# Kernel optimization log

Hardware: AMD Instinct MI355X
Metric: run time of the kernel (lower is better)

Reference implementation:

```python
import jax, jax.numpy as jnp
import numpy as np

N_NODES = 1024
IN_FEATURES = 512
N_HEADS = 4
N_HIDDEN = 32  # out_features (128) // n_heads (4)
NEG_SLOPE = 0.2


def setup_inputs() -> dict:
    key = jax.random.key(0)
    k1, k2, k3, k4, k5 = jax.random.split(key, 5)
    h = jax.random.normal(k1, (N_NODES, IN_FEATURES), dtype=jnp.float32)
    adj_mat = jax.random.randint(k2, (N_NODES, N_NODES, 1), 0, 2, dtype=jnp.int32)
    s = 1.0 / np.sqrt(IN_FEATURES)
    W_l = jax.random.uniform(k3, (IN_FEATURES, N_HEADS * N_HIDDEN), jnp.float32, -s, s)
    W_r = jax.random.uniform(k4, (IN_FEATURES, N_HEADS * N_HIDDEN), jnp.float32, -s, s)
    sa = 1.0 / np.sqrt(N_HIDDEN)
    attn_w = jax.random.uniform(k5, (N_HIDDEN,), jnp.float32, -sa, sa)
    return {"h": h, "adj_mat": adj_mat, "W_l": W_l, "W_r": W_r, "attn_w": attn_w}


def reference(h, adj_mat, W_l, W_r, attn_w):
    # GraphAttentionV2Layer forward (eval mode: dropout = identity)
    n = h.shape[0]
    g_l = (h @ W_l).reshape(n, N_HEADS, N_HIDDEN)  # source-side (j)
    g_r = (h @ W_r).reshape(n, N_HEADS, N_HIDDEN)  # dest-side (i)
    # g_sum[i, j, h, f] = g_l[j] + g_r[i]  (repeat / repeat_interleave semantics)
    g_sum = g_l[None, :, :, :] + g_r[:, None, :, :]  # [N, N, H, hid]
    act = jnp.where(g_sum >= 0, g_sum, NEG_SLOPE * g_sum)
    e = jnp.einsum('ijhf,f->ijh', act, attn_w)  # [N, N, H]
    mask = (adj_mat == 0)  # broadcasts [N, N, 1] -> [N, N, H]
    e = jnp.where(mask, -jnp.inf, e)
    a = jax.nn.softmax(e, axis=1)  # softmax over neighbors j
    h_prime = jnp.einsum('ijh,jhf->ihf', a, g_r)  # note: aggregates g_r, per source
    h_prime = h_prime.reshape(n, N_HEADS * N_HIDDEN)  # is_concat=True
    # not output layer -> ELU activation (output dropout is identity in eval)
    out = jnp.where(h_prime > 0, h_prime, jnp.expm1(h_prime))
    return out
```

## Files before the change

### kernel.cpp

```cpp
#include <hip/hip_runtime.h>
#include <math.h>

#define N_NODES 1024
#define IN_F 512
#define N_HEADS 4
#define N_HID 32
#define OUT_F 128
#define GF 256
#define NEG_SLOPE 0.2f

__global__ __launch_bounds__(256, 2) void gat_gemm(
    const float* __restrict__ hmat, const float* __restrict__ Wl,
    const float* __restrict__ Wr, float* __restrict__ gpart,
    float* __restrict__ den)
{
  const int b = blockIdx.x;
  if (b < 16) den[b * 256 + threadIdx.x] = 0.f;
  const int kc = b & 7, ct = (b >> 3) & 3, it = b >> 5;
  const int i0 = it * 64, k0 = kc * 64, cb0 = ct * 64;
  const float* __restrict__ W = (cb0 < 128) ? (Wl + cb0) : (Wr + (cb0 - 128));

  __shared__ float As[16][68];
  __shared__ float Bs[16][64];

  const int tx = threadIdx.x & 15, ty = threadIdx.x >> 4;
  const int ar = threadIdx.x >> 2, ak = (threadIdx.x & 3) * 4;
  const int bk = threadIdx.x >> 4, bc = (threadIdx.x & 15) * 4;

  float4 acc0 = {0.f, 0.f, 0.f, 0.f}, acc1 = acc0, acc2 = acc0, acc3 = acc0;

  float4 av = *(const float4*)(hmat + (size_t)(i0 + ar) * IN_F + k0 + ak);
  float4 bv = *(const float4*)(W + (size_t)(k0 + bk) * OUT_F + bc);

  for (int t = 0; t < 64; t += 16) {
    __syncthreads();
    As[ak + 0][ar] = av.x; As[ak + 1][ar] = av.y;
    As[ak + 2][ar] = av.z; As[ak + 3][ar] = av.w;
    *(float4*)&Bs[bk][bc] = bv;
    __syncthreads();
    if (t < 48) {
      av = *(const float4*)(hmat + (size_t)(i0 + ar) * IN_F + k0 + t + 16 + ak);
      bv = *(const float4*)(W + (size_t)(k0 + t + 16 + bk) * OUT_F + bc);
    }
#pragma unroll
    for (int k = 0; k < 16; ++k) {
      const float4 a  = *(const float4*)&As[k][ty * 4];
      const float4 bb = *(const float4*)&Bs[k][tx * 4];
      acc0.x = fmaf(a.x, bb.x, acc0.x); acc0.y = fmaf(a.x, bb.y, acc0.y);
      acc0.z = fmaf(a.x, bb.z, acc0.z); acc0.w = fmaf(a.x, bb.w, acc0.w);
      acc1.x = fmaf(a.y, bb.x, acc1.x); acc1.y = fmaf(a.y, bb.y, acc1.y);
      acc1.z = fmaf(a.y, bb.z, acc1.z); acc1.w = fmaf(a.y, bb.w, acc1.w);
      acc2.x = fmaf(a.z, bb.x, acc2.x); acc2.y = fmaf(a.z, bb.y, acc2.y);
      acc2.z = fmaf(a.z, bb.z, acc2.z); acc2.w = fmaf(a.z, bb.w, acc2.w);
      acc3.x = fmaf(a.w, bb.x, acc3.x); acc3.y = fmaf(a.w, bb.y, acc3.y);
      acc3.z = fmaf(a.w, bb.z, acc3.z); acc3.w = fmaf(a.w, bb.w, acc3.w);
    }
  }
  const size_t rbase = (size_t)kc * N_NODES + i0 + ty * 4;
  const int cc = cb0 + tx * 4;
  *(float4*)(gpart + (rbase + 0) * GF + cc) = acc0;
  *(float4*)(gpart + (rbase + 1) * GF + cc) = acc1;
  *(float4*)(gpart + (rbase + 2) * GF + cc) = acc2;
  *(float4*)(gpart + (rbase + 3) * GF + cc) = acc3;
}

__global__ __launch_bounds__(256) void gat_reduceWab(
    const float* __restrict__ gpart, const float* __restrict__ attn_w,
    float* __restrict__ g, float* __restrict__ abuf, float* __restrict__ bbuf)
{
  const int tid = threadIdx.x;
  const int l = tid & 63, r = tid >> 6;
  const int row = blockIdx.x * 4 + r;
  const size_t o = (size_t)row * GF + l * 4;
  float4 s = *(const float4*)(gpart + o);
#pragma unroll
  for (int c = 1; c < 8; ++c) {
    const float4 v = *(const float4*)(gpart + (size_t)c * (N_NODES * GF) + o);
    s.x += v.x; s.y += v.y; s.z += v.z; s.w += v.w;
  }
  *(float4*)(g + o) = s;
  const float4 a4 = *(const float4*)(attn_w + (l & 7) * 4);
  float d = 0.6f * (s.x * a4.x + s.y * a4.y + s.z * a4.z + s.w * a4.w);
  d += __shfl_xor(d, 1);
  d += __shfl_xor(d, 2);
  d += __shfl_xor(d, 4);
  if ((l & 7) == 0) {
    const int hq = l >> 3;
    if (hq < 4) abuf[hq * N_NODES + row] = d;
    else        bbuf[(hq - 4) * N_NODES + row] = d;
  }
}

__global__ __launch_bounds__(256, 2) void gat_fused(
    const float* __restrict__ g, const float* __restrict__ abuf,
    const float* __restrict__ bbuf, const float* __restrict__ attn_w,
    const int* __restrict__ adj, float* __restrict__ num_part,
    float* __restrict__ den)
{
  __shared__ float4 gl_s[32 * 32];
  __shared__ float4 gr_s[32 * 32];
  __shared__ float as_[4 * 33];

  const int b = blockIdx.x;
  const int jc = b & 7, it = b >> 3;
  const int i0 = it * 16, j0 = jc * 128;

  const int tid = threadIdx.x;
  const int jg = tid & 3, hh = (tid >> 2) & 3, il = tid >> 4;
  const int i = i0 + il;

  const int srow = tid >> 3, sf4 = tid & 7, sjg = srow >> 3;

  float4 gr_i[8], c2[8];
#pragma unroll
  for (int f4 = 0; f4 < 8; ++f4) {
    gr_i[f4] = *(const float4*)(g + (size_t)i * GF + 128 + hh * N_HID + f4 * 4);
    const float4 a4 = *(const float4*)(attn_w + f4 * 4);
    c2[f4] = make_float4(0.4f * a4.x, 0.4f * a4.y, 0.4f * a4.z, 0.4f * a4.w);
  }
  const float beta = bbuf[hh * N_NODES + i];

  int slot[8], wslot[4];
#pragma unroll
  for (int f4 = 0; f4 < 8; ++f4) slot[f4] = hh * 8 + ((f4 + jg + 2 * hh) & 7);
#pragma unroll
  for (int q = 0; q < 4; ++q) wslot[q] = q * 8 + ((sf4 + sjg + 2 * q) & 7);

  float4 pgl[4], pgr[4];
  float pa = 0.f;
  {
    const float* gsrc = g + (size_t)(j0 + srow) * GF;
#pragma unroll
    for (int q = 0; q < 4; ++q) {
      pgl[q] = *(const float4*)(gsrc + (sf4 + 8 * q) * 4);
      pgr[q] = *(const float4*)(gsrc + 128 + (sf4 + 8 * q) * 4);
    }
    if (tid < 128) pa = abuf[(tid >> 5) * N_NODES + j0 + (tid & 31)];
  }

  float4 num4[8];
#pragma unroll
  for (int f4 = 0; f4 < 8; ++f4) num4[f4] = make_float4(0.f, 0.f, 0.f, 0.f);
  float den_t = 0.f;

  for (int t = 0; t < 4; ++t) {
    __syncthreads();
#pragma unroll
    for (int q = 0; q < 4; ++q) {
      gl_s[srow * 32 + wslot[q]] = pgl[q];
      gr_s[srow * 32 + wslot[q]] = pgr[q];
    }
    if (tid < 128) as_[(tid >> 5) * 33 + (tid & 31)] = pa;
    __syncthreads();
    if (t < 3) {
      const float* gs2 = g + (size_t)(j0 + (t + 1) * 32 + srow) * GF;
#pragma unroll
      for (int q = 0; q < 4; ++q) {
        pgl[q] = *(const float4*)(gs2 + (sf4 + 8 * q) * 4);
        pgr[q] = *(const float4*)(gs2 + 128 + (sf4 + 8 * q) * 4);
      }
      if (tid < 128) pa = abuf[(tid >> 5) * N_NODES + j0 + (t + 1) * 32 + (tid & 31)];
    }
    const int4 ad0 = *(const int4*)(adj + (size_t)i * N_NODES + j0 + t * 32 + jg * 8);
    const int4 ad1 = *(const int4*)(adj + (size_t)i * N_NODES + j0 + t * 32 + jg * 8 + 4);
    const int* adp0 = (const int*)&ad0;
    const int* adp1 = (const int*)&ad1;

#pragma unroll
    for (int jj = 0; jj < 8; ++jj) {
      const int jl = jg * 8 + jj;
      const float4* glrow = &gl_s[jl * 32];
      const float4* grrow = &gr_s[jl * 32];
      float4 a0 = make_float4(0.f, 0.f, 0.f, 0.f), a1 = a0;
#pragma unroll
      for (int f4 = 0; f4 < 8; f4 += 2) {
        const float4 v0 = glrow[slot[f4]];
        const float4 v1 = glrow[slot[f4 + 1]];
        float sx, sy, sz, sw;
        sx = v0.x + gr_i[f4].x; sy = v0.y + gr_i[f4].y;
        sz = v0.z + gr_i[f4].z; sw = v0.w + gr_i[f4].w;
        a0.x = fmaf(c2[f4].x, __builtin_fabsf(sx), a0.x);
        a0.y = fmaf(c2[f4].y, __builtin_fabsf(sy), a0.y);
        a0.z = fmaf(c2[f4].z, __builtin_fabsf(sz), a0.z);
        a0.w = fmaf(c2[f4].w, __builtin_fabsf(sw), a0.w);
        sx = v1.x + gr_i[f4 + 1].x; sy = v1.y + gr_i[f4 + 1].y;
        sz = v1.z + gr_i[f4 + 1].z; sw = v1.w + gr_i[f4 + 1].w;
        a1.x = fmaf(c2[f4 + 1].x, __builtin_fabsf(sx), a1.x);
        a1.y = fmaf(c2[f4 + 1].y, __builtin_fabsf(sy), a1.y);
        a1.z = fmaf(c2[f4 + 1].z, __builtin_fabsf(sz), a1.z);
        a1.w = fmaf(c2[f4 + 1].w, __builtin_fabsf(sw), a1.w);
      }
      float e = ((a0.x + a0.y) + (a0.z + a0.w)) + ((a1.x + a1.y) + (a1.z + a1.w));
      e += as_[hh * 33 + jl] + beta;
      float p = __expf(e);
      const int am = (jj < 4) ? adp0[jj] : adp1[jj - 4];
      p = am ? p : 0.f;
      den_t += p;
#pragma unroll
      for (int f4 = 0; f4 < 8; ++f4) {
        const float4 gv = grrow[slot[f4]];
        num4[f4].x = fmaf(p, gv.x, num4[f4].x);
        num4[f4].y = fmaf(p, gv.y, num4[f4].y);
        num4[f4].z = fmaf(p, gv.z, num4[f4].z);
        num4[f4].w = fmaf(p, gv.w, num4[f4].w);
      }
    }
  }

#pragma unroll
  for (int m = 1; m < 4; m <<= 1) {
    den_t += __shfl_xor(den_t, m);
#pragma unroll
    for (int f4 = 0; f4 < 8; ++f4) {
      num4[f4].x += __shfl_xor(num4[f4].x, m);
      num4[f4].y += __shfl_xor(num4[f4].y, m);
      num4[f4].z += __shfl_xor(num4[f4].z, m);
      num4[f4].w += __shfl_xor(num4[f4].w, m);
    }
  }
  if (jg == 0) {
    float* np = num_part + ((size_t)jc * N_NODES + i) * OUT_F + hh * N_HID;
#pragma unroll
    for (int f4 = 0; f4 < 8; ++f4) *(float4*)(np + f4 * 4) = num4[f4];
    atomicAdd(&den[hh * N_NODES + i], den_t);
  }
}

__global__ __launch_bounds__(256) void gat_fin(
    const float* __restrict__ num_part, const float* __restrict__ den,
    float* __restrict__ outp)
{
  const int flat = blockIdx.x * 256 + threadIdx.x;
  const int i = flat >> 7, hf = flat & 127, hh = hf >> 5;
  float t[8];
#pragma unroll
  for (int c = 0; c < 8; ++c)
    t[c] = num_part[(size_t)c * (N_NODES * OUT_F) + flat];
  float s = ((t[0] + t[1]) + (t[2] + t[3])) + ((t[4] + t[5]) + (t[6] + t[7]));
  float v = s / den[hh * N_NODES + i];
  outp[flat] = v > 0.f ? v : expm1f(v);
}

extern "C" void kernel_launch(void* const* d_in, const int* in_sizes, int n_in,
                              void* d_out, int out_size, void* d_ws, size_t ws_size,
                              hipStream_t stream) {
  const float* hmat  = (const float*)d_in[0];
  const int*   adj   = (const int*)d_in[1];
  const float* Wl    = (const float*)d_in[2];
  const float* Wr    = (const float*)d_in[3];
  const float* attnw = (const float*)d_in[4];
  float* outp = (float*)d_out;

  char* ws = (char*)d_ws;
  float* gpart = (float*)(ws);
  float* g     = (float*)(ws + (8u << 20));
  float* den   = (float*)(ws + (9u << 20));
  float* abuf  = (float*)(ws + (9u << 20) + (64u << 10));
  float* bbuf  = (float*)(ws + (9u << 20) + (128u << 10));
  float* npart = (float*)(ws + (10u << 20));

  gat_gemm<<<512, 256, 0, stream>>>(hmat, Wl, Wr, gpart, den);
  gat_reduceWab<<<256, 256, 0, stream>>>(gpart, attnw, g, abuf, bbuf);
  gat_fused<<<512, 256, 0, stream>>>(g, abuf, bbuf, attnw, adj, npart, den);
  gat_fin<<<512, 256, 0, stream>>>(npart, den, outp);
}
```

Before: 126.3 us.

## Pack adjacency into bitmasks and restructure fused attention tiling with per-chunk denominators

Adds a pre-pass that packs the int32 adjacency matrix into 64-bit ballot bitmasks, so the fused kernel reads one word per row chunk instead of int4 loads. The fused kernel is retiled to 32 rows by 64 columns across 16 column chunks. Each thread now covers half of one head's features, with a cross-lane shuffle to complete the score. Denominator atomics are replaced by per-chunk partial sums reduced in the final kernel, which removes the zeroing from the GEMM. The cost is an extra kernel launch and doubled partial-numerator traffic in the finalize step.

```diff
diff --git a/kernel.cpp b/kernel.cpp
--- a/kernel.cpp
+++ b/kernel.cpp
@@ -9,13 +9,25 @@
 #define GF 256
 #define NEG_SLOPE 0.2f
 
+__global__ __launch_bounds__(256) void gat_pack(
+    const int* __restrict__ adj, unsigned long long* __restrict__ bits)
+{
+  const int i = blockIdx.x;
+  const int t = threadIdx.x;
+#pragma unroll
+  for (int q = 0; q < 4; ++q) {
+    const int j = q * 256 + t;
+    const int a = adj[(size_t)i * N_NODES + j];
+    const unsigned long long m = __ballot(a != 0);
+    if ((t & 63) == 0) bits[i * 16 + (j >> 6)] = m;
+  }
+}
+
 __global__ __launch_bounds__(256, 2) void gat_gemm(
     const float* __restrict__ hmat, const float* __restrict__ Wl,
-    const float* __restrict__ Wr, float* __restrict__ gpart,
-    float* __restrict__ den)
+    const float* __restrict__ Wr, float* __restrict__ gpart)
 {
   const int b = blockIdx.x;
-  if (b < 16) den[b * 256 + threadIdx.x] = 0.f;
   const int kc = b & 7, ct = (b >> 3) & 3, it = b >> 5;
   const int i0 = it * 64, k0 = kc * 64, cb0 = ct * 64;
   const float* __restrict__ W = (cb0 < 128) ? (Wl + cb0) : (Wr + (cb0 - 128));
@@ -92,152 +104,111 @@
 }
 
 __global__ __launch_bounds__(256, 2) void gat_fused(
-    const float* __restrict__ g, const float* __restrict__ abuf,
-    const float* __restrict__ bbuf, const float* __restrict__ attn_w,
-    const int* __restrict__ adj, float* __restrict__ num_part,
-    float* __restrict__ den)
-{
-  __shared__ float4 gl_s[32 * 32];
-  __shared__ float4 gr_s[32 * 32];
-  __shared__ float as_[4 * 33];
+    const float* __restrict__ g, const float* __restrict__ attn_w,
+    const float* __restrict__ abuf, const float* __restrict__ bbuf,
+    const unsigned long long* __restrict__ bits,
+    float* __restrict__ num_part, float* __restrict__ den_part)
+{
+  __shared__ float T[32 * 132];
+  __shared__ float as_[4 * 17];
 
   const int b = blockIdx.x;
-  const int jc = b & 7, it = b >> 3;
-  const int i0 = it * 16, j0 = jc * 128;
-
-  const int tid = threadIdx.x;
-  const int jg = tid & 3, hh = (tid >> 2) & 3, il = tid >> 4;
+  const int jc = b & 15, it = b >> 4;
+  const int i0 = it * 32, j0 = jc * 64;
+
+  const int t = threadIdx.x;
+  const int hh = t >> 6, half = (t >> 5) & 1, il = t & 31;
   const int i = i0 + il;
-
-  const int srow = tid >> 3, sf4 = tid & 7, sjg = srow >> 3;
-
-  float4 gr_i[8], c2[8];
-#pragma unroll
-  for (int f4 = 0; f4 < 8; ++f4) {
-    gr_i[f4] = *(const float4*)(g + (size_t)i * GF + 128 + hh * N_HID + f4 * 4);
-    const float4 a4 = *(const float4*)(attn_w + f4 * 4);
-    c2[f4] = make_float4(0.4f * a4.x, 0.4f * a4.y, 0.4f * a4.z, 0.4f * a4.w);
+  const int fbase = hh * N_HID + half * 16;
+
+  float4 gri[4], c2[4], num4[4];
+#pragma unroll
+  for (int q = 0; q < 4; ++q) {
+    gri[q] = *(const float4*)(g + (size_t)i * GF + 128 + fbase + q * 4);
+    const float4 a4 = *(const float4*)(attn_w + half * 16 + q * 4);
+    c2[q] = make_float4(0.4f * a4.x, 0.4f * a4.y, 0.4f * a4.z, 0.4f * a4.w);
+    num4[q] = make_float4(0.f, 0.f, 0.f, 0.f);
   }
   const float beta = bbuf[hh * N_NODES + i];
-
-  int slot[8], wslot[4];
-#pragma unroll
-  for (int f4 = 0; f4 < 8; ++f4) slot[f4] = hh * 8 + ((f4 + jg + 2 * hh) & 7);
-#pragma unroll
-  for (int q = 0; q < 4; ++q) wslot[q] = q * 8 + ((sf4 + sjg + 2 * q) & 7);
-
-  float4 pgl[4], pgr[4];
-  float pa = 0.f;
+  const unsigned long long bm = bits[(size_t)i * 16 + jc];
+  float den_t = 0.f;
+
+  const int sr = t >> 4, sc = t & 15;
+
+  for (int ts = 0; ts < 4; ++ts) {
+    __syncthreads();
+    {
+      const float* src = g + (size_t)(j0 + ts * 16 + sr) * GF + sc * 16;
+      float* dst = &T[sr * 260 + sc * 16];
+#pragma unroll
+      for (int k = 0; k < 4; ++k)
+        *(float4*)(dst + k * 4) = *(const float4*)(src + k * 4);
+      if (t < 64)
+        as_[(t >> 4) * 17 + (t & 15)] =
+            abuf[(t >> 4) * N_NODES + j0 + ts * 16 + (t & 15)];
+    }
+    __syncthreads();
+    const unsigned int w16 = (unsigned int)(bm >> (ts * 16)) & 0xFFFFu;
+#pragma unroll
+    for (int jj = 0; jj < 16; ++jj) {
+      const float* row = &T[jj * 260];
+      float part = 0.f;
+      float4 grq[4];
+#pragma unroll
+      for (int q = 0; q < 4; ++q) {
+        const float4 gl = *(const float4*)(row + fbase + q * 4);
+        grq[q] = *(const float4*)(row + 128 + fbase + q * 4);
+        float s;
+        s = gl.x + gri[q].x; part = fmaf(c2[q].x, __builtin_fabsf(s), part);
+        s = gl.y + gri[q].y; part = fmaf(c2[q].y, __builtin_fabsf(s), part);
+        s = gl.z + gri[q].z; part = fmaf(c2[q].z, __builtin_fabsf(s), part);
+        s = gl.w + gri[q].w; part = fmaf(c2[q].w, __builtin_fabsf(s), part);
+      }
+      const float full = part + __shfl_xor(part, 32);
+      const float e = full + as_[hh * 17 + jj] + beta;
+      const float p = ((w16 >> jj) & 1u) ? __expf(e) : 0.f;
+      den_t += p;
+#pragma unroll
+      for (int q = 0; q < 4; ++q) {
+        num4[q].x = fmaf(p, grq[q].x, num4[q].x);
+        num4[q].y = fmaf(p, grq[q].y, num4[q].y);
+        num4[q].z = fmaf(p, grq[q].z, num4[q].z);
+        num4[q].w = fmaf(p, grq[q].w, num4[q].w);
+      }
+    }
+  }
+
+  if (half == 0)
+    den_part[((size_t)jc * N_HEADS + hh) * N_NODES + i] = den_t;
+
+  __syncthreads();
+#pragma unroll
+  for (int q = 0; q < 4; ++q)
+    *(float4*)&T[il * 132 + fbase + q * 4] = num4[q];
+  __syncthreads();
   {
-    const float* gsrc = g + (size_t)(j0 + srow) * GF;
-#pragma unroll
-    for (int q = 0; q < 4; ++q) {
-      pgl[q] = *(const float4*)(gsrc + (sf4 + 8 * q) * 4);
-      pgr[q] = *(const float4*)(gsrc + 128 + (sf4 + 8 * q) * 4);
-    }
-    if (tid < 128) pa = abuf[(tid >> 5) * N_NODES + j0 + (tid & 31)];
-  }
-
-  float4 num4[8];
-#pragma unroll
-  for (int f4 = 0; f4 < 8; ++f4) num4[f4] = make_float4(0.f, 0.f, 0.f, 0.f);
-  float den_t = 0.f;
-
-  for (int t = 0; t < 4; ++t) {
-    __syncthreads();
-#pragma unroll
-    for (int q = 0; q < 4; ++q) {
-      gl_s[srow * 32 + wslot[q]] = pgl[q];
-      gr_s[srow * 32 + wslot[q]] = pgr[q];
-    }
-    if (tid < 128) as_[(tid >> 5) * 33 + (tid & 31)] = pa;
-    __syncthreads();
-    if (t < 3) {
-      const float* gs2 = g + (size_t)(j0 + (t + 1) * 32 + srow) * GF;
-#pragma unroll
-      for (int q = 0; q < 4; ++q) {
-        pgl[q] = *(const float4*)(gs2 + (sf4 + 8 * q) * 4);
-        pgr[q] = *(const float4*)(gs2 + 128 + (sf4 + 8 * q) * 4);
-      }
-      if (tid < 128) pa = abuf[(tid >> 5) * N_NODES + j0 + (t + 1) * 32 + (tid & 31)];
-    }
-    const int4 ad0 = *(const int4*)(adj + (size_t)i * N_NODES + j0 + t * 32 + jg * 8);
-    const int4 ad1 = *(const int4*)(adj + (size_t)i * N_NODES + j0 + t * 32 + jg * 8 + 4);
-    const int* adp0 = (const int*)&ad0;
-    const int* adp1 = (const int*)&ad1;
-
-#pragma unroll
-    for (int jj = 0; jj < 8; ++jj) {
-      const int jl = jg * 8 + jj;
-      const float4* glrow = &gl_s[jl * 32];
-      const float4* grrow = &gr_s[jl * 32];
-      float4 a0 = make_float4(0.f, 0.f, 0.f, 0.f), a1 = a0;
-#pragma unroll
-      for (int f4 = 0; f4 < 8; f4 += 2) {
-        const float4 v0 = glrow[slot[f4]];
-        const float4 v1 = glrow[slot[f4 + 1]];
-        float sx, sy, sz, sw;
-        sx = v0.x + gr_i[f4].x; sy = v0.y + gr_i[f4].y;
-        sz = v0.z + gr_i[f4].z; sw = v0.w + gr_i[f4].w;
-        a0.x = fmaf(c2[f4].x, __builtin_fabsf(sx), a0.x);
-        a0.y = fmaf(c2[f4].y, __builtin_fabsf(sy), a0.y);
-        a0.z = fmaf(c2[f4].z, __builtin_fabsf(sz), a0.z);
-        a0.w = fmaf(c2[f4].w, __builtin_fabsf(sw), a0.w);
-        sx = v1.x + gr_i[f4 + 1].x; sy = v1.y + gr_i[f4 + 1].y;
-        sz = v1.z + gr_i[f4 + 1].z; sw = v1.w + gr_i[f4 + 1].w;
-        a1.x = fmaf(c2[f4 + 1].x, __builtin_fabsf(sx), a1.x);
-        a1.y = fmaf(c2[f4 + 1].y, __builtin_fabsf(sy), a1.y);
-        a1.z = fmaf(c2[f4 + 1].z, __builtin_fabsf(sz), a1.z);
-        a1.w = fmaf(c2[f4 + 1].w, __builtin_fabsf(sw), a1.w);
-      }
-      float e = ((a0.x + a0.y) + (a0.z + a0.w)) + ((a1.x + a1.y) + (a1.z + a1.w));
-      e += as_[hh * 33 + jl] + beta;
-      float p = __expf(e);
-      const int am = (jj < 4) ? adp0[jj] : adp1[jj - 4];
-      p = am ? p : 0.f;
-      den_t += p;
-#pragma unroll
-      for (int f4 = 0; f4 < 8; ++f4) {
-        const float4 gv = grrow[slot[f4]];
-        num4[f4].x = fmaf(p, gv.x, num4[f4].x);
-        num4[f4].y = fmaf(p, gv.y, num4[f4].y);
-        num4[f4].z = fmaf(p, gv.z, num4[f4].z);
-        num4[f4].w = fmaf(p, gv.w, num4[f4].w);
-      }
-    }
-  }
-
-#pragma unroll
-  for (int m = 1; m < 4; m <<= 1) {
-    den_t += __shfl_xor(den_t, m);
-#pragma unroll
-    for (int f4 = 0; f4 < 8; ++f4) {
-      num4[f4].x += __shfl_xor(num4[f4].x, m);
-      num4[f4].y += __shfl_xor(num4[f4].y, m);
-      num4[f4].z += __shfl_xor(num4[f4].z, m);
-      num4[f4].w += __shfl_xor(num4[f4].w, m);
-    }
-  }
-  if (jg == 0) {
-    float* np = num_part + ((size_t)jc * N_NODES + i) * OUT_F + hh * N_HID;
-#pragma unroll
-    for (int f4 = 0; f4 < 8; ++f4) *(float4*)(np + f4 * 4) = num4[f4];
-    atomicAdd(&den[hh * N_NODES + i], den_t);
+    const int r = t >> 3, cg = t & 7;
+    float* dst = num_part + ((size_t)jc * N_NODES + i0 + r) * OUT_F + cg * 16;
+    const float* srcl = &T[r * 132 + cg * 16];
+#pragma unroll
+    for (int k = 0; k < 4; ++k)
+      *(float4*)(dst + k * 4) = *(const float4*)(srcl + k * 4);
   }
 }
 
 __global__ __launch_bounds__(256) void gat_fin(
-    const float* __restrict__ num_part, const float* __restrict__ den,
+    const float* __restrict__ num_part, const float* __restrict__ den_part,
     float* __restrict__ outp)
 {
   const int flat = blockIdx.x * 256 + threadIdx.x;
   const int i = flat >> 7, hf = flat & 127, hh = hf >> 5;
-  float t[8];
-#pragma unroll
-  for (int c = 0; c < 8; ++c)
-    t[c] = num_part[(size_t)c * (N_NODES * OUT_F) + flat];
-  float s = ((t[0] + t[1]) + (t[2] + t[3])) + ((t[4] + t[5]) + (t[6] + t[7]));
-  float v = s / den[hh * N_NODES + i];
+  float s = 0.f, d = 0.f;
+#pragma unroll
+  for (int c = 0; c < 16; ++c) {
+    s += num_part[(size_t)c * (N_NODES * OUT_F) + flat];
+    d += den_part[((size_t)c * N_HEADS + hh) * N_NODES + i];
+  }
+  const float v = s / d;
   outp[flat] = v > 0.f ? v : expm1f(v);
 }
 
@@ -254,13 +225,16 @@
   char* ws = (char*)d_ws;
   float* gpart = (float*)(ws);
   float* g     = (float*)(ws + (8u << 20));
-  float* den   = (float*)(ws + (9u << 20));
-  float* abuf  = (float*)(ws + (9u << 20) + (64u << 10));
-  float* bbuf  = (float*)(ws + (9u << 20) + (128u << 10));
-  float* npart = (float*)(ws + (10u << 20));
-
-  gat_gemm<<<512, 256, 0, stream>>>(hmat, Wl, Wr, gpart, den);
+  float* abuf  = (float*)(ws + (9u << 20));
+  float* bbuf  = (float*)(ws + (9u << 20) + (64u << 10));
+  unsigned long long* bits =
+      (unsigned long long*)(ws + (9u << 20) + (128u << 10));
+  float* denp  = (float*)(ws + (9u << 20) + (256u << 10));
+  float* nump  = (float*)(ws + (10u << 20));
+
+  gat_pack<<<1024, 256, 0, stream>>>(adj, bits);
+  gat_gemm<<<512, 256, 0, stream>>>(hmat, Wl, Wr, gpart);
   gat_reduceWab<<<256, 256, 0, stream>>>(gpart, attnw, g, abuf, bbuf);
-  gat_fused<<<512, 256, 0, stream>>>(g, abuf, bbuf, attnw, adj, npart, den);
-  gat_fin<<<512, 256, 0, stream>>>(npart, den, outp);
-}
+  gat_fused<<<512, 256, 0, stream>>>(g, attnw, abuf, bbuf, bits, nump, denp);
+  gat_fin<<<512, 256, 0, stream>>>(nump, denp, outp);
+}
```

Result: slower. 147.2 us (+16.5%).
